# Optimization experiments

Measured on AMD Instinct MI355X. Metric: run time of the kernel, lower is better.

The kernel has to match this reference:

```python
import jax, jax.numpy as jnp
import numpy as np

N, E, B = 50000, 600000, 64
ANN, D, STEPS, ETYPES, CLS = 64, 128, 5, 4, 10


def setup_inputs() -> dict:
    key = jax.random.key(0)
    ks = jax.random.split(key, 12)
    return {
        "annotation": jax.random.normal(ks[0], (N, ANN), jnp.float32),
        "src": jax.random.randint(ks[1], (E,), 0, N),
        "dst": jax.random.randint(ks[2], (E,), 0, N),
        "etypes": jax.random.randint(ks[3], (E,), 0, ETYPES),
        "node2graph": jnp.sort(jax.random.randint(ks[4], (N,), 0, B)),
        "labels": jax.random.randint(ks[5], (B,), 0, CLS),
        "W_lin": jax.random.normal(ks[6], (ETYPES, D, D), jnp.float32) / np.sqrt(D),
        "b_lin": jnp.zeros((ETYPES, D), jnp.float32),
        "W_ih": jax.random.normal(ks[7], (3 * D, D), jnp.float32) / np.sqrt(D),
        "W_hh": jax.random.normal(ks[8], (3 * D, D), jnp.float32) / np.sqrt(D),
        "b_ih": jnp.zeros((3 * D,), jnp.float32),
        "b_hh": jnp.zeros((3 * D,), jnp.float32),
        "gate_w": jax.random.normal(ks[9], (1, ANN + D), jnp.float32) / np.sqrt(ANN + D),
        "gate_b": jnp.zeros((1,), jnp.float32),
        "out_w": jax.random.normal(ks[10], (CLS, ANN + D), jnp.float32) / np.sqrt(ANN + D),
        "out_b": jnp.zeros((CLS,), jnp.float32),
    }


def reference(annotation, src, dst, etypes, node2graph, labels,
              W_lin, b_lin, W_ih, W_hh, b_ih, b_hh,
              gate_w, gate_b, out_w, out_b):
    n = annotation.shape[0]
    d = W_lin.shape[-1]
    nb = labels.shape[0]
    # h1 = [annotation | zeros]  -> [N, D]
    h = jnp.concatenate(
        [annotation, jnp.zeros((n, d - annotation.shape[1]), annotation.dtype)], -1)

    def step(hc, _):
        # per-edge-type linear transform of all nodes: [K, N, D]
        all_t = jnp.einsum('nd,kod->kno', hc, W_lin) + b_lin[:, None, :]
        m = all_t[etypes, src]                                  # [E, D] messages
        a = jax.ops.segment_sum(m, dst, num_segments=n)         # [N, D] aggregate
        # torch GRUCell: gates ordered (reset, update, new)
        gi = a @ W_ih.T + b_ih
        gh = hc @ W_hh.T + b_hh
        i_r, i_z, i_n = jnp.split(gi, 3, axis=-1)
        h_r, h_z, h_n = jnp.split(gh, 3, axis=-1)
        r = jax.nn.sigmoid(i_r + h_r)
        z = jax.nn.sigmoid(i_z + h_z)
        nt = jnp.tanh(i_n + r * h_n)
        return (1.0 - z) * nt + z * hc, None

    h, _ = jax.lax.scan(step, h, None, length=STEPS)
    feat = jnp.concatenate([h, annotation], -1)                 # [N, D+ANN]
    # global attention pooling: segment softmax over nodes per graph
    gate = (feat @ gate_w.T + gate_b)[:, 0]                     # [N]
    gmax = jax.ops.segment_max(gate, node2graph, num_segments=nb)
    ex = jnp.exp(gate - gmax[node2graph])
    denom = jax.ops.segment_sum(ex, node2graph, num_segments=nb)
    alpha = ex / denom[node2graph]
    readout = jax.ops.segment_sum(feat * alpha[:, None], node2graph, num_segments=nb)
    logits = readout @ out_w.T + out_b                          # [B, CLS]
    preds = jnp.argmax(logits, -1)
    logp = jax.nn.log_softmax(logits, -1)
    loss = -jnp.mean(jnp.take_along_axis(logp, labels[:, None], axis=1))
    return loss, preds
```

## Files before the change

### kernel.cpp

```cpp
#include <hip/hip_runtime.h>
#include <math.h>

#define DD 128
#define ANND 64
#define NSTEPS 5
#define NTYPES 4
#define NCLS 10

typedef __attribute__((ext_vector_type(8))) short short8v;
typedef __attribute__((ext_vector_type(4))) float f32x4;

__device__ __forceinline__ void split2(float x, unsigned short& hi, unsigned short& lo) {
  unsigned u = __float_as_uint(x);
  unsigned hb = (u + 0x7FFFu + ((u >> 16) & 1u)) >> 16;
  hi = (unsigned short)hb;
  float r = x - __uint_as_float(hb << 16);
  unsigned v = __float_as_uint(r);
  lo = (unsigned short)((v + 0x7FFFu + ((v >> 16) & 1u)) >> 16);
}

__device__ __forceinline__ float bf2f(unsigned short u) {
  return __uint_as_float(((unsigned)u) << 16);
}
__device__ __forceinline__ float lo16f(unsigned u) { return __uint_as_float(u << 16); }
__device__ __forceinline__ float hi16f(unsigned u) { return __uint_as_float(u & 0xffff0000u); }

__device__ __forceinline__ void gload16(const unsigned short* g, unsigned short* l) {
  __builtin_amdgcn_global_load_lds(
      (const __attribute__((address_space(1))) unsigned int*)(const void*)g,
      (__attribute__((address_space(3))) unsigned int*)(void*)l, 16, 0, 0);
}

__global__ void k_init(const float* __restrict__ ann,
    unsigned short* __restrict__ hI, int n, int npad) {
  int idx = blockIdx.x * blockDim.x + threadIdx.x;
  if (idx >= npad * DD) return;
  int node = idx >> 7, d = idx & 127;
  float v = (node < n && d < ANND) ? ann[node * ANND + d] : 0.0f;
  unsigned short hi, lo; split2(v, hi, lo);
  hI[(size_t)node * 256 + d] = hi;
  hI[(size_t)node * 256 + 128 + d] = lo;
}

__global__ void k_deg4(const int* __restrict__ dst, const int* __restrict__ et,
    int* __restrict__ deg4, int e) {
  int i = blockIdx.x * blockDim.x + threadIdx.x;
  if (i < e) atomicAdd(&deg4[dst[i] * 4 + et[i]], 1);
}

__global__ __launch_bounds__(1024) void k_scan(const int* __restrict__ deg4,
    int* __restrict__ base, int n) {
  __shared__ int part[1024];
  int t = threadIdx.x;
  int chunk = (n + 1023) >> 10;
  int s = t * chunk, e = min(n, s + chunk);
  int sum = 0;
  for (int i = s; i < e; ++i) {
    const int4 d4 = *(const int4*)(deg4 + (size_t)i * 4);
    sum += d4.x + d4.y + d4.z + d4.w;
  }
  part[t] = sum;
  __syncthreads();
  int own = sum;
  for (int off = 1; off < 1024; off <<= 1) {
    int v = (t >= off) ? part[t - off] : 0;
    __syncthreads();
    part[t] += v;
    __syncthreads();
  }
  int run = part[t] - own;
  for (int i = s; i < e; ++i) {
    base[i] = run;
    const int4 d4 = *(const int4*)(deg4 + (size_t)i * 4);
    run += d4.x + d4.y + d4.z + d4.w;
  }
  if (s < n && e == n) base[n] = run;
}

__global__ void k_place(const int* __restrict__ src, const int* __restrict__ dst,
    const int* __restrict__ et, const int* __restrict__ base, int* __restrict__ cursor,
    int* __restrict__ cpack, int e) {
  int i = blockIdx.x * blockDim.x + threadIdx.x;
  if (i >= e) return;
  int d = dst[i];
  int pos = base[d] + atomicAdd(&cursor[d], 1);
  cpack[pos] = src[i] | (et[i] << 18);
}

__global__ void k_aggh(const uint2* __restrict__ hI2, const int* __restrict__ base,
    const int* __restrict__ cpack, unsigned short* __restrict__ A3hi,
    unsigned short* __restrict__ A3lo, int nbase, int cc) {
  int w = threadIdx.x >> 6;
  int lane = threadIdx.x & 63;
  int local = blockIdx.x * 4 + w;
  if (local >= cc) return;
  int node = nbase + local;
  int s = base[node], e = base[node + 1];
  float4 a0 = make_float4(0.f,0.f,0.f,0.f), a1 = a0, a2 = a0, a3 = a0;
  for (int t0 = s; t0 < e; t0 += 64) {
    int cnt = min(64, e - t0);
    int mypk = (t0 + lane < e) ? cpack[t0 + lane] : 0;
    int i = 0;
    for (; i + 8 <= cnt; i += 8) {
      int pk[8]; uint2 v[8];
      #pragma unroll
      for (int j = 0; j < 8; ++j) pk[j] = __shfl(mypk, i + j);
      #pragma unroll
      for (int j = 0; j < 8; ++j) v[j] = hI2[(size_t)(pk[j] & 0x3ffff) * 64 + lane];
      #pragma unroll
      for (int j = 0; j < 8; ++j) {
        float f0 = lo16f(v[j].x), f1 = hi16f(v[j].x);
        float f2 = lo16f(v[j].y), f3 = hi16f(v[j].y);
        int t = pk[j] >> 18;
        if (t == 0)      { a0.x += f0; a0.y += f1; a0.z += f2; a0.w += f3; }
        else if (t == 1) { a1.x += f0; a1.y += f1; a1.z += f2; a1.w += f3; }
        else if (t == 2) { a2.x += f0; a2.y += f1; a2.z += f2; a2.w += f3; }
        else             { a3.x += f0; a3.y += f1; a3.z += f2; a3.w += f3; }
      }
    }
    for (; i < cnt; ++i) {
      int pk = __shfl(mypk, i);
      uint2 vv = hI2[(size_t)(pk & 0x3ffff) * 64 + lane];
      float f0 = lo16f(vv.x), f1 = hi16f(vv.x), f2 = lo16f(vv.y), f3 = hi16f(vv.y);
      int t = pk >> 18;
      if (t == 0)      { a0.x += f0; a0.y += f1; a0.z += f2; a0.w += f3; }
      else if (t == 1) { a1.x += f0; a1.y += f1; a1.z += f2; a1.w += f3; }
      else if (t == 2) { a2.x += f0; a2.y += f1; a2.z += f2; a2.w += f3; }
      else             { a3.x += f0; a3.y += f1; a3.z += f2; a3.w += f3; }
    }
  }
  a0.x += __shfl_down(a0.x, 32); a0.y += __shfl_down(a0.y, 32);
  a0.z += __shfl_down(a0.z, 32); a0.w += __shfl_down(a0.w, 32);
  a1.x += __shfl_down(a1.x, 32); a1.y += __shfl_down(a1.y, 32);
  a1.z += __shfl_down(a1.z, 32); a1.w += __shfl_down(a1.w, 32);
  a2.x += __shfl_down(a2.x, 32); a2.y += __shfl_down(a2.y, 32);
  a2.z += __shfl_down(a2.z, 32); a2.w += __shfl_down(a2.w, 32);
  a3.x += __shfl_down(a3.x, 32); a3.y += __shfl_down(a3.y, 32);
  a3.z += __shfl_down(a3.z, 32); a3.w += __shfl_down(a3.w, 32);
  if (lane < 32) {
    ushort4* A3h4 = (ushort4*)A3hi;
    ushort4* A3l4 = (ushort4*)A3lo;
    size_t b4 = (size_t)local * 128 + lane;
    ushort4 h4, l4;
    split2(a0.x, h4.x, l4.x); split2(a0.y, h4.y, l4.y);
    split2(a0.z, h4.z, l4.z); split2(a0.w, h4.w, l4.w);
    A3h4[b4] = h4; A3l4[b4] = l4;
    split2(a1.x, h4.x, l4.x); split2(a1.y, h4.y, l4.y);
    split2(a1.z, h4.z, l4.z); split2(a1.w, h4.w, l4.w);
    A3h4[b4 + 32] = h4; A3l4[b4 + 32] = l4;
    split2(a2.x, h4.x, l4.x); split2(a2.y, h4.y, l4.y);
    split2(a2.z, h4.z, l4.z); split2(a2.w, h4.w, l4.w);
    A3h4[b4 + 64] = h4; A3l4[b4 + 64] = l4;
    split2(a3.x, h4.x, l4.x); split2(a3.y, h4.y, l4.y);
    split2(a3.z, h4.z, l4.z); split2(a3.w, h4.w, l4.w);
    A3h4[b4 + 96] = h4; A3l4[b4 + 96] = l4;
  }
}

__global__ void k_fusew(const float* __restrict__ Wih, const float* __restrict__ Wlin,
    float* __restrict__ VW) {
  int idx = blockIdx.x * blockDim.x + threadIdx.x;
  if (idx >= 384 * 512) return;
  int c = idx >> 9, kd = idx & 511;
  int k = kd >> 7, d = kd & 127;
  const float* wi = Wih + (size_t)c * DD;
  const float* wl = Wlin + (size_t)k * DD * DD + d;
  float s = 0.f;
  for (int o = 0; o < DD; ++o) s += wi[o] * wl[(size_t)o * DD];
  VW[idx] = s;
}

__global__ void k_wbig(const float* __restrict__ VW, const float* __restrict__ Whh,
    unsigned short* __restrict__ WbH, unsigned short* __restrict__ WbL) {
  int idx = blockIdx.x * blockDim.x + threadIdx.x;
  if (idx >= 512 * 640) return;
  int c = idx / 640, k = idx % 640;
  float v;
  if (c < 256)      v = (k < 512) ? VW[(size_t)c * 512 + k] : Whh[(size_t)c * DD + (k - 512)];
  else if (c < 384) v = (k < 512) ? VW[(size_t)c * 512 + k] : 0.f;
  else              v = (k < 512) ? 0.f : Whh[(size_t)(c - 128) * DD + (k - 512)];
  int g = c >> 7, d = c & 127;
  int cn = ((d >> 5) << 7) + (((d >> 4) & 1) << 6) + (g << 4) + (d & 15);
  unsigned short h, l; split2(v, h, l);
  WbH[(size_t)cn * 640 + k] = h;
  WbL[(size_t)cn * 640 + k] = l;
}

__global__ void k_fuseb(const float* __restrict__ Wih, const float* __restrict__ bih,
    const float* __restrict__ bhh, const float* __restrict__ blin,
    float* __restrict__ bias_big, float* __restrict__ cb4) {
  int c = blockIdx.x * blockDim.x + threadIdx.x;
  if (c >= 512) return;
  float b;
  if (c < 256) b = bih[c] + bhh[c];
  else if (c < 384) b = bih[c];
  else b = bhh[c - 128];
  bias_big[c] = b;
  for (int k = 0; k < NTYPES; ++k) {
    float s = 0.f;
    if (c < 384) {
      const float* wi = Wih + (size_t)c * DD;
      const float* bl = blin + (size_t)k * DD;
      for (int o = 0; o < DD; ++o) s += wi[o] * bl[o];
    }
    cb4[k * 512 + c] = s;
  }
}

__global__ __launch_bounds__(256) void k_gru8(
    const unsigned short* __restrict__ A3hi, const unsigned short* __restrict__ A3lo,
    const unsigned short* __restrict__ HI, const unsigned short* __restrict__ WbH,
    const unsigned short* __restrict__ WbL, const float* __restrict__ bias_big,
    const float* __restrict__ cb4, const int* __restrict__ deg4,
    unsigned short* __restrict__ OI, int nbase, int cc) {
  __shared__ unsigned short ldsX[4096];
  __shared__ unsigned short ldsW[12288];
  int tid = threadIdx.x;
  int wc = tid >> 6, lane = tid & 63;
  int lr = lane & 15, lk = lane >> 4;
  int rowbase = blockIdx.y * 64;
  int ytile = blockIdx.x;
  int wtb = ytile * 256;
  f32x4 acc[4][4];
  #pragma unroll
  for (int mm = 0; mm < 4; ++mm)
    #pragma unroll
    for (int g = 0; g < 4; ++g) acc[mm][g] = (f32x4){0.f, 0.f, 0.f, 0.f};

  int srow = tid >> 2, sc0 = tid & 3;
  int xcs = sc0 ^ ((srow >> 1) & 3);
  int wwb = (tid & ~63) * 8;

  for (int it = 0; it < 20; ++it) {
    int k0 = it * 32;
    __syncthreads();
    {
      const unsigned short *xsH, *xsL;
      if (k0 < 512) {
        size_t off = (size_t)(rowbase + srow) * 512 + k0 + xcs * 8;
        xsH = A3hi + off; xsL = A3lo + off;
      } else {
        size_t off = (size_t)(nbase + rowbase + srow) * 256 + (k0 - 512) + xcs * 8;
        xsH = HI + off; xsL = HI + off + 128;
      }
      gload16(xsH, ldsX + wwb);
      gload16(xsL, ldsX + 2048 + wwb);
    }
    int skip = (k0 < 512) ? 3 : 2;
    #pragma unroll
    for (int i2 = 0; i2 < 3; ++i2) {
      int rc = i2 * 64 + srow;
      int grp = rc / 48, rem = rc - grp * 48;
      int s = rem >> 4, w16 = rem & 15;
      int g = s + (s >= skip ? 1 : 0);
      int srcrow = grp * 64 + g * 16 + w16;
      int wcs = sc0 ^ ((rc >> 1) & 3);
      size_t woff = (size_t)(wtb + srcrow) * 640 + k0 + wcs * 8;
      unsigned short* wdst = ldsW + i2 * 2048 + wwb;
      gload16(WbH + woff, wdst);
      gload16(WbL + woff, wdst + 6144);
    }
    __syncthreads();

    int nnSkip = skip;
    short8v xh[4], xl[4];
    #pragma unroll
    for (int mm = 0; mm < 4; ++mm) {
      int r = mm * 16 + lr;
      int a = r * 32 + ((lk ^ ((r >> 1) & 3)) << 3);
      xh[mm] = *(const short8v*)(ldsX + a);
      xl[mm] = *(const short8v*)(ldsX + 2048 + a);
    }
    #pragma unroll
    for (int nn = 0; nn < 4; ++nn) {
      if (nn == nnSkip) continue;
      int s = nn - (nn > nnSkip ? 1 : 0);
      int rc = wc * 48 + s * 16 + lr;
      int a = rc * 32 + ((lk ^ ((rc >> 1) & 3)) << 3);
      short8v wh = *(const short8v*)(ldsW + a);
      short8v wl = *(const short8v*)(ldsW + 6144 + a);
      #pragma unroll
      for (int mm = 0; mm < 4; ++mm) {
        acc[mm][nn] = __builtin_amdgcn_mfma_f32_16x16x32_bf16(xh[mm], wh, acc[mm][nn], 0, 0, 0);
        acc[mm][nn] = __builtin_amdgcn_mfma_f32_16x16x32_bf16(xh[mm], wl, acc[mm][nn], 0, 0, 0);
        acc[mm][nn] = __builtin_amdgcn_mfma_f32_16x16x32_bf16(xl[mm], wh, acc[mm][nn], 0, 0, 0);
      }
    }
  }

  int d = ytile * 64 + wc * 16 + lr;
  float bsr = bias_big[d], bsz = bias_big[128 + d];
  float bgn = bias_big[256 + d], bhn = bias_big[384 + d];
  float cbr[4], cbz[4], cbn[4];
  #pragma unroll
  for (int k = 0; k < 4; ++k) {
    cbr[k] = cb4[k * 512 + d];
    cbz[k] = cb4[k * 512 + 128 + d];
    cbn[k] = cb4[k * 512 + 256 + d];
  }
  #pragma unroll
  for (int mm = 0; mm < 4; ++mm) {
    #pragma unroll
    for (int j = 0; j < 4; ++j) {
      int row = rowbase + mm * 16 + lk * 4 + j;
      if (row < cc) {
        int4 dg = *(const int4*)(deg4 + (size_t)row * 4);
        float s_r = acc[mm][0][j] + bsr + dg.x * cbr[0] + dg.y * cbr[1] + dg.z * cbr[2] + dg.w * cbr[3];
        float s_z = acc[mm][1][j] + bsz + dg.x * cbz[0] + dg.y * cbz[1] + dg.z * cbz[2] + dg.w * cbz[3];
        float g_n = acc[mm][2][j] + bgn + dg.x * cbn[0] + dg.y * cbn[1] + dg.z * cbn[2] + dg.w * cbn[3];
        float h_n = acc[mm][3][j] + bhn;
        float r = 1.f / (1.f + expf(-s_r));
        float z = 1.f / (1.f + expf(-s_z));
        float nt = tanhf(g_n + r * h_n);
        size_t hb = (size_t)(nbase + row) * 256 + d;
        float hold = bf2f(HI[hb]) + bf2f(HI[hb + 128]);
        float hv = (1.f - z) * nt + z * hold;
        unsigned short uh, ul; split2(hv, uh, ul);
        OI[hb] = uh; OI[hb + 128] = ul;
      }
    }
  }
}

__global__ void k_gate(const unsigned short* __restrict__ hI, const float* __restrict__ ann,
    const float* __restrict__ gw, const float* __restrict__ gb,
    float* __restrict__ gate, int n) {
  int gt = blockIdx.x * blockDim.x + threadIdx.x;
  int wv = gt >> 6;
  int lane = threadIdx.x & 63;
  if (wv >= n) return;
  size_t b = (size_t)wv * 256;
  float h0 = bf2f(hI[b + lane]) + bf2f(hI[b + 128 + lane]);
  float h1 = bf2f(hI[b + 64 + lane]) + bf2f(hI[b + 192 + lane]);
  float p = h0 * gw[lane] + h1 * gw[64 + lane]
          + ann[(size_t)wv * ANND + lane] * gw[128 + lane];
  for (int off = 32; off; off >>= 1) p += __shfl_down(p, off);
  if (lane == 0) gate[wv] = p + gb[0];
}

__global__ void k_bounds(const int* __restrict__ n2g, int* __restrict__ startg,
    int* __restrict__ endg, int n) {
  int i = blockIdx.x * blockDim.x + threadIdx.x;
  if (i >= n) return;
  int g = n2g[i];
  if (i == 0 || n2g[i - 1] != g) startg[g] = i;
  if (i == n - 1 || n2g[i + 1] != g) endg[g] = i + 1;
}

__global__ __launch_bounds__(256) void k_mden(const float* __restrict__ gate,
    const int* __restrict__ startg, const int* __restrict__ endg,
    float* __restrict__ mg, float* __restrict__ invg) {
  __shared__ float red[256];
  int g = blockIdx.x;
  int s = startg[g], e = endg[g];
  int tid = threadIdx.x;
  float m = -1e30f;
  for (int i = s + tid; i < e; i += 256) m = fmaxf(m, gate[i]);
  red[tid] = m; __syncthreads();
  for (int off = 128; off; off >>= 1) {
    if (tid < off) red[tid] = fmaxf(red[tid], red[tid + off]);
    __syncthreads();
  }
  m = red[0];
  __syncthreads();
  float sum = 0.f;
  for (int i = s + tid; i < e; i += 256) sum += expf(gate[i] - m);
  red[tid] = sum; __syncthreads();
  for (int off = 128; off; off >>= 1) {
    if (tid < off) red[tid] += red[tid + off];
    __syncthreads();
  }
  if (tid == 0) { mg[g] = m; invg[g] = (s < e) ? 1.f / red[0] : 0.f; }
}

__global__ __launch_bounds__(256) void k_pool2(const float* __restrict__ gate,
    const unsigned* __restrict__ hIU, const float* __restrict__ ann,
    const int* __restrict__ startg, const int* __restrict__ endg,
    const float* __restrict__ mg, const float* __restrict__ invg,
    float* __restrict__ readout) {
  __shared__ float redx[256], redy[256];
  int g = blockIdx.x;
  int s = startg[g], e = endg[g];
  int nl = threadIdx.x >> 6, lane = threadIdx.x & 63;
  float m = mg[g], inv = invg[g];
  if (blockIdx.y == 0) {
    float ax = 0.f, ay = 0.f;
    for (int i = s + nl; i < e; i += 4) {
      float al = expf(gate[i] - m) * inv;
      unsigned uh = hIU[(size_t)i * 128 + lane];
      unsigned ul = hIU[(size_t)i * 128 + 64 + lane];
      ax += al * (lo16f(uh) + lo16f(ul));
      ay += al * (hi16f(uh) + hi16f(ul));
    }
    redx[threadIdx.x] = ax; redy[threadIdx.x] = ay;
    __syncthreads();
    if (nl == 0) {
      float sx = redx[lane] + redx[64 + lane] + redx[128 + lane] + redx[192 + lane];
      float sy = redy[lane] + redy[64 + lane] + redy[128 + lane] + redy[192 + lane];
      readout[g * (DD + ANND) + 2 * lane] = sx;
      readout[g * (DD + ANND) + 2 * lane + 1] = sy;
    }
  } else {
    float acc = 0.f;
    for (int i = s + nl; i < e; i += 4) {
      float al = expf(gate[i] - m) * inv;
      acc += al * ann[(size_t)i * ANND + lane];
    }
    redx[threadIdx.x] = acc;
    __syncthreads();
    if (nl == 0)
      readout[g * (DD + ANND) + DD + lane] =
          redx[lane] + redx[64 + lane] + redx[128 + lane] + redx[192 + lane];
  }
}

__global__ void k_logits(const float* __restrict__ readout, const float* __restrict__ ow,
    const float* __restrict__ ob, const int* __restrict__ labels,
    float* __restrict__ out, int B) {
  __shared__ float lsum[64];
  int g = threadIdx.x;
  float loss_c = 0.f;
  if (g < B) {
    float lg[NCLS];
    float mx = -1e30f;
    int best = 0;
    for (int c = 0; c < NCLS; ++c) {
      float acc = ob[c];
      const float* r = readout + g * (DD + ANND);
      const float* w = ow + c * (DD + ANND);
      for (int d = 0; d < DD + ANND; ++d) acc += r[d] * w[d];
      lg[c] = acc;
      if (acc > mx) { mx = acc; best = c; }
    }
    float se = 0.f;
    for (int c = 0; c < NCLS; ++c) se += expf(lg[c] - mx);
    float lse = mx + logf(se);
    loss_c = -(lg[labels[g]] - lse);
    out[1 + g] = (float)best;
  }
  lsum[threadIdx.x] = loss_c;
  __syncthreads();
  for (int off = 32; off; off >>= 1) {
    if (threadIdx.x < off) lsum[threadIdx.x] += lsum[threadIdx.x + off];
    __syncthreads();
  }
  if (threadIdx.x == 0) out[0] = lsum[0] / (float)B;
}

extern "C" void kernel_launch(void* const* d_in, const int* in_sizes, int n_in,
                              void* d_out, int out_size, void* d_ws, size_t ws_size,
                              hipStream_t stream) {
  const float* annotation = (const float*)d_in[0];
  const int*   src        = (const int*)d_in[1];
  const int*   dst        = (const int*)d_in[2];
  const int*   et         = (const int*)d_in[3];
  const int*   n2g        = (const int*)d_in[4];
  const int*   labels     = (const int*)d_in[5];
  const float* W_lin      = (const float*)d_in[6];
  const float* b_lin      = (const float*)d_in[7];
  const float* W_ih       = (const float*)d_in[8];
  const float* W_hh       = (const float*)d_in[9];
  const float* b_ih       = (const float*)d_in[10];
  const float* b_hh       = (const float*)d_in[11];
  const float* gate_w     = (const float*)d_in[12];
  const float* gate_b     = (const float*)d_in[13];
  const float* out_w      = (const float*)d_in[14];
  const float* out_b      = (const float*)d_in[15];

  int N = in_sizes[0] / ANND;
  int E = in_sizes[1];
  int B = in_sizes[5];
  int Np = (N + 127) & ~127;

  auto rup = [](size_t b) { return (b + 255) & ~(size_t)255; };
  size_t fixed = 0;
  fixed += 2 * rup((size_t)Np * 512);
  fixed += rup((size_t)N * 4);
  fixed += rup((size_t)B * (DD + ANND) * 4);
  fixed += 4 * rup((size_t)B * 4);
  fixed += rup((size_t)(N + 1) * 4);
  fixed += rup((size_t)N * 4);
  fixed += rup((size_t)N * 16);
  fixed += rup((size_t)E * 4);
  fixed += rup(384 * 512 * 4);
  fixed += 2 * rup(512 * 640 * 2);
  fixed += rup(512 * 4) + rup(4 * 512 * 4);
  size_t slack = 1 << 20;
  size_t avail = (ws_size > fixed + slack) ? ws_size - fixed - slack : 0;
  long long ch = (long long)(avail / 2048);
  int CH = (int)((ch / 128) * 128);
  if (CH < 128) CH = 128;
  if (CH > Np) CH = Np;

  char* wsP = (char*)d_ws;
  auto alloc = [&](size_t bytes) -> void* {
    void* p = (void*)wsP;
    wsP += (bytes + 255) & ~(size_t)255;
    return p;
  };
  unsigned short* hP[2];
  hP[0] = (unsigned short*)alloc((size_t)Np * 512);
  hP[1] = (unsigned short*)alloc((size_t)Np * 512);
  float* gate = (float*)alloc((size_t)N * 4);
  float* readout = (float*)alloc((size_t)B * (DD + ANND) * 4);
  int* startg = (int*)alloc((size_t)B * 4);
  int* endg   = (int*)alloc((size_t)B * 4);
  float* mg   = (float*)alloc((size_t)B * 4);
  float* invg = (float*)alloc((size_t)B * 4);
  int* base   = (int*)alloc((size_t)(N + 1) * 4);
  int* cursor = (int*)alloc((size_t)N * 4);
  int* deg4   = (int*)alloc((size_t)N * 16);
  int* cpack  = (int*)alloc((size_t)E * 4);
  float* VW   = (float*)alloc(384 * 512 * 4);
  unsigned short* WbH = (unsigned short*)alloc(512 * 640 * 2);
  unsigned short* WbL = (unsigned short*)alloc(512 * 640 * 2);
  float* bias_big = (float*)alloc(512 * 4);
  float* cb4  = (float*)alloc(4 * 512 * 4);
  unsigned short* A3hi = (unsigned short*)alloc((size_t)CH * 512 * 2);
  unsigned short* A3lo = (unsigned short*)alloc((size_t)CH * 512 * 2);

  k_init<<<(Np * DD + 255) / 256, 256, 0, stream>>>(annotation, hP[0], N, Np);
  hipMemsetAsync(cursor, 0, (size_t)N * 4, stream);
  hipMemsetAsync(deg4, 0, (size_t)N * 16, stream);
  hipMemsetAsync(startg, 0x7f, (size_t)B * 4, stream);
  hipMemsetAsync(endg, 0, (size_t)B * 4, stream);
  k_deg4<<<(E + 255) / 256, 256, 0, stream>>>(dst, et, deg4, E);
  k_scan<<<1, 1024, 0, stream>>>(deg4, base, N);
  k_place<<<(E + 255) / 256, 256, 0, stream>>>(src, dst, et, base, cursor, cpack, E);
  k_bounds<<<(N + 255) / 256, 256, 0, stream>>>(n2g, startg, endg, N);
  k_fusew<<<(384 * 512 + 255) / 256, 256, 0, stream>>>(W_ih, W_lin, VW);
  k_wbig<<<(512 * 640 + 255) / 256, 256, 0, stream>>>(VW, W_hh, WbH, WbL);
  k_fuseb<<<2, 256, 0, stream>>>(W_ih, b_ih, b_hh, b_lin, bias_big, cb4);

  int cur = 0;
  for (int s = 0; s < NSTEPS; ++s) {
    int nxt = cur ^ 1;
    for (int nbase = 0; nbase < N; nbase += CH) {
      int cc = min(CH, N - nbase);
      int cgrid = (cc + 63) / 64;
      k_aggh<<<(cc + 3) / 4, 256, 0, stream>>>(
          (const uint2*)hP[cur], base, cpack, A3hi, A3lo, nbase, cc);
      k_gru8<<<dim3(2, cgrid), 256, 0, stream>>>(A3hi, A3lo,
          hP[cur], WbH, WbL, bias_big, cb4,
          deg4 + (size_t)nbase * 4, hP[nxt], nbase, cc);
    }
    cur ^= 1;
  }

  k_gate<<<(N * 64 + 255) / 256, 256, 0, stream>>>(
      hP[cur], annotation, gate_w, gate_b, gate, N);
  k_mden<<<B, 256, 0, stream>>>(gate, startg, endg, mg, invg);
  k_pool2<<<dim3(B, 2), 256, 0, stream>>>(gate, (const unsigned*)hP[cur],
      annotation, startg, endg, mg, invg, readout);
  k_logits<<<1, 64, 0, stream>>>(readout, out_w, out_b, labels, (float*)d_out, B);
}
```

Before: 1.178 ms.

## Merge GRU column tiles into one 512-thread block per row tile

```diff
diff --git a/kernel.cpp b/kernel.cpp
--- a/kernel.cpp
+++ b/kernel.cpp
@@ -207,58 +207,58 @@
   }
 }
 
-__global__ __launch_bounds__(256) void k_gru8(
+__global__ __launch_bounds__(512) void k_gru9(
     const unsigned short* __restrict__ A3hi, const unsigned short* __restrict__ A3lo,
     const unsigned short* __restrict__ HI, const unsigned short* __restrict__ WbH,
     const unsigned short* __restrict__ WbL, const float* __restrict__ bias_big,
     const float* __restrict__ cb4, const int* __restrict__ deg4,
     unsigned short* __restrict__ OI, int nbase, int cc) {
   __shared__ unsigned short ldsX[4096];
-  __shared__ unsigned short ldsW[12288];
+  __shared__ unsigned short ldsW[24576];
   int tid = threadIdx.x;
-  int wc = tid >> 6, lane = tid & 63;
+  int wid = tid >> 6, lane = tid & 63;
   int lr = lane & 15, lk = lane >> 4;
-  int rowbase = blockIdx.y * 64;
-  int ytile = blockIdx.x;
-  int wtb = ytile * 256;
+  int rowbase = blockIdx.x * 64;
   f32x4 acc[4][4];
   #pragma unroll
   for (int mm = 0; mm < 4; ++mm)
     #pragma unroll
     for (int g = 0; g < 4; ++g) acc[mm][g] = (f32x4){0.f, 0.f, 0.f, 0.f};
 
-  int srow = tid >> 2, sc0 = tid & 3;
-  int xcs = sc0 ^ ((srow >> 1) & 3);
-  int wwb = (tid & ~63) * 8;
+  int xplane = wid >> 2;
+  int xrow = (wid & 3) * 16 + (lane >> 2);
+  int xgc = (lane & 3) ^ ((xrow >> 1) & 3);
+  unsigned short* xdst = ldsX + xplane * 2048 + (wid & 3) * 512;
 
   for (int it = 0; it < 20; ++it) {
     int k0 = it * 32;
     __syncthreads();
     {
-      const unsigned short *xsH, *xsL;
+      const unsigned short* xs;
       if (k0 < 512) {
-        size_t off = (size_t)(rowbase + srow) * 512 + k0 + xcs * 8;
-        xsH = A3hi + off; xsL = A3lo + off;
+        size_t off = (size_t)(rowbase + xrow) * 512 + k0 + xgc * 8;
+        xs = (xplane == 0 ? A3hi : A3lo) + off;
       } else {
-        size_t off = (size_t)(nbase + rowbase + srow) * 256 + (k0 - 512) + xcs * 8;
-        xsH = HI + off; xsL = HI + off + 128;
+        size_t off = (size_t)(nbase + rowbase + xrow) * 256 + (k0 - 512) + xplane * 128 + xgc * 8;
+        xs = HI + off;
       }
-      gload16(xsH, ldsX + wwb);
-      gload16(xsL, ldsX + 2048 + wwb);
+      gload16(xs, xdst);
     }
     int skip = (k0 < 512) ? 3 : 2;
     #pragma unroll
-    for (int i2 = 0; i2 < 3; ++i2) {
-      int rc = i2 * 64 + srow;
+    for (int p = 0; p < 6; ++p) {
+      int plane = (p >= 3) ? 1 : 0;
+      int pp = p - plane * 3;
+      int rc = pp * 128 + wid * 16 + (lane >> 2);
+      int gc = (lane & 3) ^ ((rc >> 1) & 3);
       int grp = rc / 48, rem = rc - grp * 48;
       int s = rem >> 4, w16 = rem & 15;
       int g = s + (s >= skip ? 1 : 0);
       int srcrow = grp * 64 + g * 16 + w16;
-      int wcs = sc0 ^ ((rc >> 1) & 3);
-      size_t woff = (size_t)(wtb + srcrow) * 640 + k0 + wcs * 8;
-      unsigned short* wdst = ldsW + i2 * 2048 + wwb;
-      gload16(WbH + woff, wdst);
-      gload16(WbL + woff, wdst + 6144);
+      size_t woff = (size_t)srcrow * 640 + k0 + gc * 8;
+      const unsigned short* wsrc = (plane ? WbL : WbH) + woff;
+      unsigned short* wdst = ldsW + plane * 12288 + pp * 4096 + wid * 512;
+      gload16(wsrc, wdst);
     }
     __syncthreads();
 
@@ -275,10 +275,10 @@
     for (int nn = 0; nn < 4; ++nn) {
       if (nn == nnSkip) continue;
       int s = nn - (nn > nnSkip ? 1 : 0);
-      int rc = wc * 48 + s * 16 + lr;
+      int rc = wid * 48 + s * 16 + lr;
       int a = rc * 32 + ((lk ^ ((rc >> 1) & 3)) << 3);
       short8v wh = *(const short8v*)(ldsW + a);
-      short8v wl = *(const short8v*)(ldsW + 6144 + a);
+      short8v wl = *(const short8v*)(ldsW + 12288 + a);
       #pragma unroll
       for (int mm = 0; mm < 4; ++mm) {
         acc[mm][nn] = __builtin_amdgcn_mfma_f32_16x16x32_bf16(xh[mm], wh, acc[mm][nn], 0, 0, 0);
@@ -288,7 +288,7 @@
     }
   }
 
-  int d = ytile * 64 + wc * 16 + lr;
+  int d = wid * 16 + lr;
   float bsr = bias_big[d], bsz = bias_big[128 + d];
   float bgn = bias_big[256 + d], bhn = bias_big[384 + d];
   float cbr[4], cbz[4], cbn[4];
@@ -540,7 +540,7 @@
       int cgrid = (cc + 63) / 64;
       k_aggh<<<(cc + 3) / 4, 256, 0, stream>>>(
           (const uint2*)hP[cur], base, cpack, A3hi, A3lo, nbase, cc);
-      k_gru8<<<dim3(2, cgrid), 256, 0, stream>>>(A3hi, A3lo,
+      k_gru9<<<cgrid, 512, 0, stream>>>(A3hi, A3lo,
           hP[cur], WbH, WbL, bias_big, cb4,
           deg4 + (size_t)nbase * 4, hP[nxt], nbase, cc);
     }
```

Result: slower. 1.496 ms (+27.1%).
